# Optimization experiments

Measured on AMD Instinct MI355X. Metric: run time of the kernel, lower is better.

Reference implementation:

```python
import jax, jax.numpy as jnp
import numpy as np

B, S, D, H = 4, 1024, 1024, 16
DH = D // H  # head dim 64
DFF = 4 * D


def _lin(x, w, b):
    # torch nn.Linear: x @ W^T + b, W: [out, in]
    return x @ w.T + b


def _heads(x):
    # [B,S,D] -> [B,H,S,DH]
    b, s, _ = x.shape
    return x.reshape(b, s, H, DH).transpose(0, 2, 1, 3)


def setup_inputs() -> dict:
    key = jax.random.key(0)
    ks = iter(jax.random.split(key, 32))

    def w(shape):
        return jax.random.normal(next(ks), shape, jnp.float32) * 0.02

    inp = {
        "global_feat": jax.random.normal(next(ks), (B, S, D), jnp.float32),
        "local_feat": jax.random.normal(next(ks), (B, S, D), jnp.float32),
        "text_feat": jax.random.normal(next(ks), (B, S, D), jnp.float32),
    }
    # embedding blocks (build) and all projections: D x D linears
    for name in ["ge", "le1", "le2", "qg", "kg", "vg", "qp", "kp", "vp", "dense", "ml"]:
        inp[name + "_w"] = w((D, D))
        inp[name + "_b"] = w((D,))
    # MLP: D -> 4D -> D
    inp["fc1_w"] = w((DFF, D)); inp["fc1_b"] = w((DFF,))
    inp["fc2_w"] = w((D, DFF)); inp["fc2_b"] = w((D,))
    return inp


def reference(global_feat, local_feat, text_feat,
              ge_w, ge_b, le1_w, le1_b, le2_w, le2_b,
              qg_w, qg_b, kg_w, kg_b, vg_w, vg_b,
              qp_w, qp_b, kp_w, kp_b, vp_w, vp_b,
              dense_w, dense_b, ml_w, ml_b,
              fc1_w, fc1_b, fc2_w, fc2_b):
    b, s, d = global_feat.shape
    scale = 1.0 / jnp.sqrt(jnp.asarray(DH, global_feat.dtype))

    # embeddings (build blocks; dropout = identity in eval)
    dup_local = _lin(local_feat, le1_w, le1_b)
    local = _lin(local_feat, le2_w, le2_b)
    glob = _lin(global_feat, ge_w, ge_b)

    # global branch: Q from global, K/V from local
    qg = _heads(_lin(glob, qg_w, qg_b))
    kg = _heads(_lin(local, kg_w, kg_b))
    vg = _heads(_lin(local, vg_w, vg_b))
    # local branch: Q from duplicated local, K/V from text
    qp = _heads(_lin(dup_local, qp_w, qp_b))
    kp = _heads(_lin(text_feat, kp_w, kp_b))
    vp = _heads(_lin(text_feat, vp_w, vp_b))

    glb_probs = jax.nn.softmax(jnp.einsum("bhqd,bhkd->bhqk", qg, kg) * scale, axis=-1)
    plb_probs = jax.nn.softmax(jnp.einsum("bhqd,bhkd->bhqk", qp, kp) * scale, axis=-1)

    # bridge: probs @ probs (the non-standard O(S^3) stage)
    plb_enh = jnp.einsum("bhqk,bhks->bhqs", glb_probs, plb_probs)

    glb_ctx = jnp.einsum("bhqk,bhkd->bhqd", glb_probs, vg)
    plb_ctx = jnp.einsum("bhqs,bhsd->bhqd", plb_enh, vp)

    def merge(x):
        return x.transpose(0, 2, 1, 3).reshape(b, s, d)

    last = merge(glb_ctx) + merge(plb_ctx)
    out = _lin(last, dense_w, dense_b)
    # MLP: D -> 4D -> D with GELU
    out = _lin(jax.nn.gelu(_lin(out, fc1_w, fc1_b), approximate=False), fc2_w, fc2_b)
    out = _lin(out, ml_w, ml_b)
    return out
```

## Files before the change

kernel.cpp:

```cpp
#include <hip/hip_runtime.h>
#include <cstdint>
#include <cstddef>

#define B_   4
#define S_   1024
#define D_   1024
#define H_   16
#define DH_  64
#define DFF_ 4096
#define M_   (B_ * S_)

typedef __bf16 bf16x8 __attribute__((ext_vector_type(8)));
typedef float  f32x4  __attribute__((ext_vector_type(4)));

__device__ __forceinline__ unsigned short f2bf(float f) {
  unsigned int u = __float_as_uint(f);
  u = (u + 0x7fffu + ((u >> 16) & 1u)) >> 16;
  return (unsigned short)u;
}

__device__ __forceinline__ float bf2f(unsigned short h) {
  return __uint_as_float(((unsigned int)h) << 16);
}

__device__ __forceinline__ void gload_lds16(const void* g, void* l) {
  __builtin_amdgcn_global_load_lds((const __attribute__((address_space(1))) void*)g,
                                   (__attribute__((address_space(3))) void*)l, 16, 0, 0);
}

#define NCVT 16
struct CvtB { const float* s[NCVT]; unsigned short* d[NCVT]; int n[NCVT]; };

__global__ __launch_bounds__(256)
void cvt_k(CvtB cb) {
  const int z = blockIdx.y;
  const float* __restrict__ s = cb.s[z];
  unsigned short* __restrict__ d = cb.d[z];
  const int n = cb.n[z];
  const int stride = gridDim.x * 256 * 4;
  for (int i = (blockIdx.x * 256 + threadIdx.x) * 4; i < n; i += stride) {
    const float4 v = *(const float4*)(s + i);
    const unsigned int a = (unsigned int)f2bf(v.x) | ((unsigned int)f2bf(v.y) << 16);
    const unsigned int b = (unsigned int)f2bf(v.z) | ((unsigned int)f2bf(v.w) << 16);
    *(uint2*)(d + i) = make_uint2(a, b);
  }
}

#define MAXB 6
struct GemmB {
  const unsigned short* A[MAXB];
  const unsigned short* W[MAXB];
  const float*          bias[MAXB];
  void*                 Y[MAXB];
};

template <int GELU, int OUTF32>
__global__ __launch_bounds__(256)
void mgemm(GemmB gb, int M, int N, int K) {
  __shared__ unsigned short sA0[128][32], sA1[128][32];
  __shared__ unsigned short sB0[128][32], sB1[128][32];

  const int z = blockIdx.z;
  const unsigned short* __restrict__ A = gb.A[z];
  const unsigned short* __restrict__ W = gb.W[z];
  const float* __restrict__ bias = gb.bias[z];

  const int t  = threadIdx.x;
  const int ln = t & 63;
  const int wv = t >> 6;
  const int wr = wv >> 1;
  const int wc = wv & 1;

  const int gx   = gridDim.x;
  const int nwg  = gx * gridDim.y;
  const int orig = blockIdx.y * gx + blockIdx.x;
  const int q8   = nwg >> 3, r8 = nwg & 7;
  const int xcd  = orig & 7, idx = orig >> 3;
  const int wgid = (xcd < r8 ? xcd * (q8 + 1) : r8 * (q8 + 1) + (xcd - r8) * q8) + idx;
  const int m0 = (wgid / gx) * 128;
  const int n0 = (wgid % gx) * 128;

  const int srow  = ln >> 2;
  const int skoff = (ln & 3) << 3;

  f32x4 acc[4][4] = {};

  char* a0 = (char*)&sA0[0][0];  char* a1 = (char*)&sA1[0][0];
  char* b0 = (char*)&sB0[0][0];  char* b1 = (char*)&sB1[0][0];

  const int rsel = ln & 15;
  const int csel = (ln >> 4) << 4;

  auto stage = [&](int kt, char* dstA, char* dstB) {
    const int k0 = kt << 5;
#pragma unroll
    for (int i = 0; i < 2; ++i) {
      const int c = (wv << 1) | i;
      gload_lds16(A + (size_t)(m0 + (c << 4) + srow) * K + k0 + skoff, dstA + (c << 10));
      gload_lds16(W + (size_t)(n0 + (c << 4) + srow) * K + k0 + skoff, dstB + (c << 10));
    }
  };

  auto compute = [&](const char* srcA, const char* srcB) {
    bf16x8 av[4], bv[4];
#pragma unroll
    for (int m = 0; m < 4; ++m)
      av[m] = *(const bf16x8*)(srcA + (((wr << 6) + (m << 4) + rsel) << 6) + csel);
#pragma unroll
    for (int n = 0; n < 4; ++n)
      bv[n] = *(const bf16x8*)(srcB + (((wc << 6) + (n << 4) + rsel) << 6) + csel);
#pragma unroll
    for (int m = 0; m < 4; ++m)
#pragma unroll
      for (int n = 0; n < 4; ++n)
        acc[m][n] = __builtin_amdgcn_mfma_f32_16x16x32_bf16(av[m], bv[n], acc[m][n], 0, 0, 0);
  };

  const int NK = K >> 5;
  stage(0, a0, b0);
  for (int kt = 0; kt < NK; kt += 2) {
    __syncthreads();
    stage(kt + 1, a1, b1);
    compute(a0, b0);
    __syncthreads();
    if (kt + 2 < NK) stage(kt + 2, a0, b0);
    compute(a1, b1);
  }

  const int rbase = m0 + (wr << 6) + ((ln >> 4) << 2);
  const int cb0   = n0 + (wc << 6) + (ln & 15);
#pragma unroll
  for (int m = 0; m < 4; ++m) {
#pragma unroll
    for (int n = 0; n < 4; ++n) {
      const int col = cb0 + (n << 4);
      const float bi = bias[col];
#pragma unroll
      for (int j = 0; j < 4; ++j) {
        const int row = rbase + (m << 4) + j;
        float x = acc[m][n][j] + bi;
        if (GELU) x = 0.5f * x * (1.0f + erff(x * 0.70710678118654752f));
        if (OUTF32) ((float*)gb.Y[z])[(size_t)row * N + col] = x;
        else        ((unsigned short*)gb.Y[z])[(size_t)row * N + col] = f2bf(x);
      }
    }
  }
}

__global__ __launch_bounds__(256)
void vtrans_k(const unsigned short* __restrict__ V, unsigned short* __restrict__ Vt) {
  const int t   = threadIdx.x;
  const int d   = t & 63;
  const int sub = t >> 6;
  const int bh  = blockIdx.y;
  const int b   = bh >> 4;
  const int col0 = (bh & 15) * DH_;
  const int kv0 = blockIdx.x * 32 + sub * 8;
  unsigned short tmp[8];
#pragma unroll
  for (int i = 0; i < 8; ++i)
    tmp[i] = V[((size_t)b * S_ + kv0 + i) * D_ + col0 + d];
  *(uint4*)(Vt + ((size_t)bh * DH_ + d) * S_ + kv0) = *(const uint4*)tmp;
}

__global__ __launch_bounds__(256)
void attn_mfma_k(const unsigned short* __restrict__ Q,
                 const unsigned short* __restrict__ K,
                 const unsigned short* __restrict__ Vt,
                 const unsigned short* __restrict__ addend,
                 unsigned short* __restrict__ O) {
  __shared__ unsigned short sQ[64 * 64];
  __shared__ unsigned short sK[64 * 64];
  __shared__ unsigned short sV[64 * 64];
  __shared__ unsigned short sP[4][16 * 72];

  const int t  = threadIdx.x;
  const int l  = t & 63;
  const int w  = t >> 6;
  const int bh = blockIdx.y;
  const int b  = bh >> 4;
  const size_t rowQ = (size_t)b * S_ + blockIdx.x * 64;
  const size_t rowK = (size_t)b * S_;
  const int col0 = (bh & 15) * DH_;

  const int lr8 = l >> 3;
  const int lsw = (l & 7) ^ lr8;
  char* sQb = (char*)sQ;
  char* sKb = (char*)sK;
  char* sVb = (char*)sV;

#pragma unroll
  for (int i = 0; i < 2; ++i) {
    const int r = w * 16 + i * 8 + lr8;
    gload_lds16(Q + (rowQ + r) * D_ + col0 + lsw * 8, sQb + w * 2048 + i * 1024);
    gload_lds16(K + (rowK + r) * D_ + col0 + lsw * 8, sKb + w * 2048 + i * 1024);
    gload_lds16(Vt + ((size_t)bh * DH_ + r) * S_ + lsw * 8, sVb + w * 2048 + i * 1024);
  }
  __syncthreads();

  bf16x8 qa[2];
#pragma unroll
  for (int c = 0; c < 2; ++c)
    qa[c] = *(const bf16x8*)(sQb + (w * 16 + (l & 15)) * 128 +
                             ((((c << 2) + (l >> 4)) ^ (l & 7)) << 4));

  f32x4 o[4] = {};
  float mrow[4] = {-1e30f, -1e30f, -1e30f, -1e30f};
  float lrow[4] = {0.f, 0.f, 0.f, 0.f};

  char* sPw = (char*)(sP[w]);

  for (int kt = 0; kt < S_ / 64; ++kt) {
    f32x4 s[4];
#pragma unroll
    for (int n = 0; n < 4; ++n) {
      f32x4 z = {};
#pragma unroll
      for (int c = 0; c < 2; ++c) {
        const bf16x8 kb = *(const bf16x8*)(sKb + (n * 16 + (l & 15)) * 128 +
                              ((((c << 2) + (l >> 4)) ^ (l & 7)) << 4));
        z = __builtin_amdgcn_mfma_f32_16x16x32_bf16(qa[c], kb, z, 0, 0, 0);
      }
      s[n] = z;
    }

#pragma unroll
    for (int j = 0; j < 4; ++j) {
      float rm = fmaxf(fmaxf(s[0][j], s[1][j]), fmaxf(s[2][j], s[3][j]));
      rm = fmaxf(rm, __shfl_xor(rm, 1));
      rm = fmaxf(rm, __shfl_xor(rm, 2));
      rm = fmaxf(rm, __shfl_xor(rm, 4));
      rm = fmaxf(rm, __shfl_xor(rm, 8));
      const float mn = fmaxf(mrow[j], rm * 0.125f);
      const float cr = __expf(mrow[j] - mn);
      mrow[j] = mn;
      float rs = 0.f;
#pragma unroll
      for (int n = 0; n < 4; ++n) {
        const float p = __expf(s[n][j] * 0.125f - mn);
        rs += p;
        ((unsigned short*)sPw)[((l >> 4) * 4 + j) * 72 + n * 16 + (l & 15)] = f2bf(p);
      }
      rs += __shfl_xor(rs, 1);
      rs += __shfl_xor(rs, 2);
      rs += __shfl_xor(rs, 4);
      rs += __shfl_xor(rs, 8);
      lrow[j] = lrow[j] * cr + rs;
#pragma unroll
      for (int n2 = 0; n2 < 4; ++n2) o[n2][j] *= cr;
    }

    bf16x8 pa[2];
#pragma unroll
    for (int kc = 0; kc < 2; ++kc)
      pa[kc] = *(const bf16x8*)(sPw + (l & 15) * 144 + kc * 64 + (l >> 4) * 16);
#pragma unroll
    for (int n2 = 0; n2 < 4; ++n2) {
#pragma unroll
      for (int kc = 0; kc < 2; ++kc) {
        const bf16x8 vb = *(const bf16x8*)(sVb + (n2 * 16 + (l & 15)) * 128 +
                               ((((kc << 2) + (l >> 4)) ^ (l & 7)) << 4));
        o[n2] = __builtin_amdgcn_mfma_f32_16x16x32_bf16(pa[kc], vb, o[n2], 0, 0, 0);
      }
    }

    __syncthreads();
    if (kt + 1 < S_ / 64) {
#pragma unroll
      for (int i = 0; i < 2; ++i) {
        const int r = w * 16 + i * 8 + lr8;
        gload_lds16(K + (rowK + (size_t)(kt + 1) * 64 + r) * D_ + col0 + lsw * 8,
                    sKb + w * 2048 + i * 1024);
        gload_lds16(Vt + ((size_t)bh * DH_ + r) * S_ + (kt + 1) * 64 + lsw * 8,
                    sVb + w * 2048 + i * 1024);
      }
    }
    __syncthreads();
  }

  float inv[4];
#pragma unroll
  for (int j = 0; j < 4; ++j) inv[j] = 1.f / lrow[j];
#pragma unroll
  for (int n2 = 0; n2 < 4; ++n2) {
#pragma unroll
    for (int j = 0; j < 4; ++j) {
      const size_t row = rowQ + w * 16 + (l >> 4) * 4 + j;
      const int col = col0 + n2 * 16 + (l & 15);
      float x = o[n2][j] * inv[j];
      if (addend != nullptr) x += bf2f(addend[row * D_ + col]);
      O[row * D_ + col] = f2bf(x);
    }
  }
}

extern "C" void kernel_launch(void* const* d_in, const int* in_sizes, int n_in,
                              void* d_out, int out_size, void* d_ws, size_t ws_size,
                              hipStream_t stream) {
  const float* gf = (const float*)d_in[0];
  const float* lf = (const float*)d_in[1];
  const float* tf = (const float*)d_in[2];
  const float* ge_w  = (const float*)d_in[3],  *ge_b  = (const float*)d_in[4];
  const float* le1_w = (const float*)d_in[5],  *le1_b = (const float*)d_in[6];
  const float* le2_w = (const float*)d_in[7],  *le2_b = (const float*)d_in[8];
  const float* qg_w  = (const float*)d_in[9],  *qg_b  = (const float*)d_in[10];
  const float* kg_w  = (const float*)d_in[11], *kg_b  = (const float*)d_in[12];
  const float* vg_w  = (const float*)d_in[13], *vg_b  = (const float*)d_in[14];
  const float* qp_w  = (const float*)d_in[15], *qp_b  = (const float*)d_in[16];
  const float* kp_w  = (const float*)d_in[17], *kp_b  = (const float*)d_in[18];
  const float* vp_w  = (const float*)d_in[19], *vp_b  = (const float*)d_in[20];
  const float* dense_w = (const float*)d_in[21], *dense_b = (const float*)d_in[22];
  const float* ml_w  = (const float*)d_in[23], *ml_b  = (const float*)d_in[24];
  const float* fc1_w = (const float*)d_in[25], *fc1_b = (const float*)d_in[26];
  const float* fc2_w = (const float*)d_in[27], *fc2_b = (const float*)d_in[28];

  float* out = (float*)d_out;

  char* p = (char*)d_ws;
  auto take = [&](size_t bytes) { char* r = p; p += (bytes + 255) & ~(size_t)255; return r; };
  const size_t WD  = (size_t)D_ * D_;
  const size_t WF  = (size_t)DFF_ * D_;
  const size_t ACT = (size_t)M_ * D_;
  const size_t HB  = (size_t)M_ * DFF_;

  unsigned short* wge    = (unsigned short*)take(WD * 2);
  unsigned short* wle1   = (unsigned short*)take(WD * 2);
  unsigned short* wle2   = (unsigned short*)take(WD * 2);
  unsigned short* wqg    = (unsigned short*)take(WD * 2);
  unsigned short* wkg    = (unsigned short*)take(WD * 2);
  unsigned short* wvg    = (unsigned short*)take(WD * 2);
  unsigned short* wqp    = (unsigned short*)take(WD * 2);
  unsigned short* wkp    = (unsigned short*)take(WD * 2);
  unsigned short* wvp    = (unsigned short*)take(WD * 2);
  unsigned short* wdense = (unsigned short*)take(WD * 2);
  unsigned short* wml    = (unsigned short*)take(WD * 2);
  unsigned short* wfc1   = (unsigned short*)take(WF * 2);
  unsigned short* wfc2   = (unsigned short*)take(WF * 2);
  unsigned short* gfb    = (unsigned short*)take(ACT * 2);
  unsigned short* lfb    = (unsigned short*)take(ACT * 2);
  unsigned short* tfb    = (unsigned short*)take(ACT * 2);
  unsigned short* glob   = (unsigned short*)take(ACT * 2);
  unsigned short* loc    = (unsigned short*)take(ACT * 2);
  unsigned short* dup    = (unsigned short*)take(ACT * 2);
  unsigned short* qgb    = (unsigned short*)take(ACT * 2);
  unsigned short* kgb    = (unsigned short*)take(ACT * 2);
  unsigned short* vgb    = (unsigned short*)take(ACT * 2);
  unsigned short* qpb    = (unsigned short*)take(ACT * 2);
  unsigned short* kpb    = (unsigned short*)take(ACT * 2);
  unsigned short* vpb    = (unsigned short*)take(ACT * 2);
  unsigned short* ub     = (unsigned short*)take(ACT * 2);
  unsigned short* lastb  = (unsigned short*)take(ACT * 2);
  unsigned short* out1   = (unsigned short*)take(ACT * 2);
  unsigned short* hbuf   = (unsigned short*)take(HB * 2);
  unsigned short* out2   = (unsigned short*)take(ACT * 2);

  unsigned short* vt1 = gfb;
  unsigned short* vtu = lfb;

  CvtB cb;
  const float* srcs[NCVT] = {ge_w, le1_w, le2_w, qg_w, kg_w, vg_w, qp_w, kp_w, vp_w,
                             dense_w, ml_w, fc1_w, fc2_w, gf, lf, tf};
  unsigned short* dsts[NCVT] = {wge, wle1, wle2, wqg, wkg, wvg, wqp, wkp, wvp,
                                wdense, wml, wfc1, wfc2, gfb, lfb, tfb};
  const int lens[NCVT] = {(int)WD,(int)WD,(int)WD,(int)WD,(int)WD,(int)WD,(int)WD,(int)WD,(int)WD,
                          (int)WD,(int)WD,(int)WF,(int)WF,(int)ACT,(int)ACT,(int)ACT};
  for (int i = 0; i < NCVT; ++i) { cb.s[i] = srcs[i]; cb.d[i] = dsts[i]; cb.n[i] = lens[i]; }
  hipLaunchKernelGGL(cvt_k, dim3(512, NCVT), dim3(256), 0, stream, cb);

  const dim3 blk(256);
  auto mkb = [](std::initializer_list<const unsigned short*> As,
                std::initializer_list<const unsigned short*> Ws,
                std::initializer_list<const float*> Bs,
                std::initializer_list<void*> Ys) {
    GemmB g{};
    int i = 0;
    auto a = As.begin(); auto w = Ws.begin(); auto b = Bs.begin(); auto y = Ys.begin();
    for (; a != As.end(); ++a, ++w, ++b, ++y, ++i) { g.A[i] = *a; g.W[i] = *w; g.bias[i] = *b; g.Y[i] = *y; }
    return g;
  };

  GemmB s1 = mkb({gfb, lfb, lfb}, {wge, wle1, wle2}, {ge_b, le1_b, le2_b},
                 {glob, dup, loc});
  hipLaunchKernelGGL((mgemm<0,0>), dim3(D_/128, M_/128, 3), blk, 0, stream, s1, M_, D_, D_);

  GemmB s2 = mkb({glob, loc, loc, dup, tfb, tfb}, {wqg, wkg, wvg, wqp, wkp, wvp},
                 {qg_b, kg_b, vg_b, qp_b, kp_b, vp_b}, {qgb, kgb, vgb, qpb, kpb, vpb});
  hipLaunchKernelGGL((mgemm<0,0>), dim3(D_/128, M_/128, 6), blk, 0, stream, s2, M_, D_, D_);

  hipLaunchKernelGGL(vtrans_k, dim3(32, 64), blk, 0, stream, vpb, vt1);
  hipLaunchKernelGGL(attn_mfma_k, dim3(16, 64), blk, 0, stream, qpb, kpb, vt1, vgb, ub);
  hipLaunchKernelGGL(vtrans_k, dim3(32, 64), blk, 0, stream, ub, vtu);
  hipLaunchKernelGGL(attn_mfma_k, dim3(16, 64), blk, 0, stream, qgb, kgb, vtu,
                     (const unsigned short*)nullptr, lastb);

  GemmB gd = mkb({lastb}, {wdense}, {dense_b}, {out1});
  hipLaunchKernelGGL((mgemm<0,0>), dim3(D_/128, M_/128, 1), blk, 0, stream, gd, M_, D_, D_);
  GemmB g1 = mkb({out1}, {wfc1}, {fc1_b}, {hbuf});
  hipLaunchKernelGGL((mgemm<1,0>), dim3(DFF_/128, M_/128, 1), blk, 0, stream, g1, M_, DFF_, D_);
  GemmB g2 = mkb({hbuf}, {wfc2}, {fc2_b}, {out2});
  hipLaunchKernelGGL((mgemm<0,0>), dim3(D_/128, M_/128, 1), blk, 0, stream, g2, M_, D_, DFF_);
  GemmB gm = mkb({out2}, {wml}, {ml_b}, {out});
  hipLaunchKernelGGL((mgemm<0,1>), dim3(D_/128, M_/128, 1), blk, 0, stream, gm, M_, D_, D_);
}
```

Before: 599.4 us.

## Fold embedding linears into projection weights and double-buffer attention K/V tiles

Since the embedding linears feed straight into the Q/K/V projections, the code now precomputes combined weights (Wq·We) with a small 1024x1024 GEMM and combined biases (Wq·be + bq). The separate 3-way embedding GEMM stage and its intermediate activations go away, so the projections read the converted input features directly. This removes a full M×D×D GEMM pass over three outputs, at the cost of a few weight-sized GEMMs, a transpose kernel and some bf16 rounding of the fused weights. The attention kernel also gets double-buffered K/V shared-memory tiles, so the next tile loads while the current one is computed.

```diff
diff --git a/kernel.cpp b/kernel.cpp
--- a/kernel.cpp
+++ b/kernel.cpp
@@ -46,6 +46,50 @@
   }
 }
 
+struct WtB { const float* s[3]; unsigned short* d[3]; };
+
+__global__ __launch_bounds__(256)
+void wtrans_k(WtB wb) {
+  const int z = blockIdx.z;
+  const float* __restrict__ S = wb.s[z];
+  unsigned short* __restrict__ T = wb.d[z];
+  const int t = threadIdx.x;
+  const int dcol = blockIdx.y * 64 + (t & 63);
+  const int r0   = blockIdx.x * 32 + (t >> 6) * 8;
+  unsigned short tmp[8];
+#pragma unroll
+  for (int i = 0; i < 8; ++i)
+    tmp[i] = f2bf(S[(size_t)(r0 + i) * 1024 + dcol]);
+  *(uint4*)(T + (size_t)dcol * 1024 + r0) = *(const uint4*)tmp;
+}
+
+struct BcB { const float* w[4]; const float* eb[4]; const float* pb[4]; float* o[4]; };
+
+__global__ __launch_bounds__(256)
+void bcomp_k(BcB bb) {
+  const int z = blockIdx.y;
+  const float* __restrict__ Wp = bb.w[z];
+  const float* __restrict__ be = bb.eb[z];
+  const float* __restrict__ pb = bb.pb[z];
+  float* __restrict__ o = bb.o[z];
+  const int w = threadIdx.x >> 6, l = threadIdx.x & 63;
+  for (int pass = 0; pass < 16; ++pass) {
+    const int n = blockIdx.x * 64 + pass * 4 + w;
+    const float* row = Wp + (size_t)n * 1024 + l * 16;
+    float acc = 0.f;
+#pragma unroll
+    for (int i = 0; i < 4; ++i) {
+      const float4 a = *(const float4*)(row + i * 4);
+      const float4 b = *(const float4*)(be + l * 16 + i * 4);
+      acc += a.x * b.x + a.y * b.y + a.z * b.z + a.w * b.w;
+    }
+    acc += __shfl_xor(acc, 1);  acc += __shfl_xor(acc, 2);
+    acc += __shfl_xor(acc, 4);  acc += __shfl_xor(acc, 8);
+    acc += __shfl_xor(acc, 16); acc += __shfl_xor(acc, 32);
+    if (l == 0) o[n] = acc + pb[n];
+  }
+}
+
 #define MAXB 6
 struct GemmB {
   const unsigned short* A[MAXB];
@@ -54,7 +98,7 @@
   void*                 Y[MAXB];
 };
 
-template <int GELU, int OUTF32>
+template <int GELU, int OUTF32, int NB>
 __global__ __launch_bounds__(256)
 void mgemm(GemmB gb, int M, int N, int K) {
   __shared__ unsigned short sA0[128][32], sA1[128][32];
@@ -134,7 +178,7 @@
 #pragma unroll
     for (int n = 0; n < 4; ++n) {
       const int col = cb0 + (n << 4);
-      const float bi = bias[col];
+      const float bi = NB ? 0.f : bias[col];
 #pragma unroll
       for (int j = 0; j < 4; ++j) {
         const int row = rbase + (m << 4) + j;
@@ -170,8 +214,8 @@
                  const unsigned short* __restrict__ addend,
                  unsigned short* __restrict__ O) {
   __shared__ unsigned short sQ[64 * 64];
-  __shared__ unsigned short sK[64 * 64];
-  __shared__ unsigned short sV[64 * 64];
+  __shared__ unsigned short sK0[64 * 64], sK1[64 * 64];
+  __shared__ unsigned short sV0[64 * 64], sV1[64 * 64];
   __shared__ unsigned short sP[4][16 * 72];
 
   const int t  = threadIdx.x;
@@ -185,43 +229,47 @@
 
   const int lr8 = l >> 3;
   const int lsw = (l & 7) ^ lr8;
-  char* sQb = (char*)sQ;
-  char* sKb = (char*)sK;
-  char* sVb = (char*)sV;
+
+  auto stageKV = [&](int kt, char* dK, char* dV) {
+#pragma unroll
+    for (int i = 0; i < 2; ++i) {
+      const int r = w * 16 + i * 8 + lr8;
+      gload_lds16(K + (rowK + (size_t)kt * 64 + r) * D_ + col0 + lsw * 8, dK + w * 2048 + i * 1024);
+      gload_lds16(Vt + ((size_t)bh * DH_ + r) * S_ + kt * 64 + lsw * 8, dV + w * 2048 + i * 1024);
+    }
+  };
 
 #pragma unroll
   for (int i = 0; i < 2; ++i) {
     const int r = w * 16 + i * 8 + lr8;
-    gload_lds16(Q + (rowQ + r) * D_ + col0 + lsw * 8, sQb + w * 2048 + i * 1024);
-    gload_lds16(K + (rowK + r) * D_ + col0 + lsw * 8, sKb + w * 2048 + i * 1024);
-    gload_lds16(Vt + ((size_t)bh * DH_ + r) * S_ + lsw * 8, sVb + w * 2048 + i * 1024);
-  }
+    gload_lds16(Q + (rowQ + r) * D_ + col0 + lsw * 8, (char*)sQ + w * 2048 + i * 1024);
+  }
+  stageKV(0, (char*)sK0, (char*)sV0);
   __syncthreads();
 
   bf16x8 qa[2];
 #pragma unroll
   for (int c = 0; c < 2; ++c)
-    qa[c] = *(const bf16x8*)(sQb + (w * 16 + (l & 15)) * 128 +
+    qa[c] = *(const bf16x8*)((char*)sQ + (w * 16 + (l & 15)) * 128 +
                              ((((c << 2) + (l >> 4)) ^ (l & 7)) << 4));
 
   f32x4 o[4] = {};
   float mrow[4] = {-1e30f, -1e30f, -1e30f, -1e30f};
   float lrow[4] = {0.f, 0.f, 0.f, 0.f};
-
   char* sPw = (char*)(sP[w]);
 
-  for (int kt = 0; kt < S_ / 64; ++kt) {
+  auto tile = [&](const char* sKb, const char* sVb) {
     f32x4 s[4];
 #pragma unroll
     for (int n = 0; n < 4; ++n) {
-      f32x4 z = {};
+      f32x4 zz = {};
 #pragma unroll
       for (int c = 0; c < 2; ++c) {
         const bf16x8 kb = *(const bf16x8*)(sKb + (n * 16 + (l & 15)) * 128 +
                               ((((c << 2) + (l >> 4)) ^ (l & 7)) << 4));
-        z = __builtin_amdgcn_mfma_f32_16x16x32_bf16(qa[c], kb, z, 0, 0, 0);
+        zz = __builtin_amdgcn_mfma_f32_16x16x32_bf16(qa[c], kb, zz, 0, 0, 0);
       }
-      s[n] = z;
+      s[n] = zz;
     }
 
 #pragma unroll
@@ -263,18 +311,14 @@
         o[n2] = __builtin_amdgcn_mfma_f32_16x16x32_bf16(pa[kc], vb, o[n2], 0, 0, 0);
       }
     }
-
+  };
+
+  for (int kt = 0; kt < S_ / 64; kt += 2) {
+    if (kt + 1 < S_ / 64) stageKV(kt + 1, (char*)sK1, (char*)sV1);
+    tile((char*)sK0, (char*)sV0);
     __syncthreads();
-    if (kt + 1 < S_ / 64) {
-#pragma unroll
-      for (int i = 0; i < 2; ++i) {
-        const int r = w * 16 + i * 8 + lr8;
-        gload_lds16(K + (rowK + (size_t)(kt + 1) * 64 + r) * D_ + col0 + lsw * 8,
-                    sKb + w * 2048 + i * 1024);
-        gload_lds16(Vt + ((size_t)bh * DH_ + r) * S_ + (kt + 1) * 64 + lsw * 8,
-                    sVb + w * 2048 + i * 1024);
-      }
-    }
+    if (kt + 2 < S_ / 64) stageKV(kt + 2, (char*)sK0, (char*)sV0);
+    tile((char*)sK1, (char*)sV1);
     __syncthreads();
   }
 
@@ -323,9 +367,6 @@
   const size_t ACT = (size_t)M_ * D_;
   const size_t HB  = (size_t)M_ * DFF_;
 
-  unsigned short* wge    = (unsigned short*)take(WD * 2);
-  unsigned short* wle1   = (unsigned short*)take(WD * 2);
-  unsigned short* wle2   = (unsigned short*)take(WD * 2);
   unsigned short* wqg    = (unsigned short*)take(WD * 2);
   unsigned short* wkg    = (unsigned short*)take(WD * 2);
   unsigned short* wvg    = (unsigned short*)take(WD * 2);
@@ -336,12 +377,20 @@
   unsigned short* wml    = (unsigned short*)take(WD * 2);
   unsigned short* wfc1   = (unsigned short*)take(WF * 2);
   unsigned short* wfc2   = (unsigned short*)take(WF * 2);
+  unsigned short* geT    = (unsigned short*)take(WD * 2);
+  unsigned short* le1T   = (unsigned short*)take(WD * 2);
+  unsigned short* le2T   = (unsigned short*)take(WD * 2);
+  unsigned short* cWqg   = (unsigned short*)take(WD * 2);
+  unsigned short* cWkg   = (unsigned short*)take(WD * 2);
+  unsigned short* cWvg   = (unsigned short*)take(WD * 2);
+  unsigned short* cWqp   = (unsigned short*)take(WD * 2);
+  float* cbqg = (float*)take(D_ * 4);
+  float* cbkg = (float*)take(D_ * 4);
+  float* cbvg = (float*)take(D_ * 4);
+  float* cbqp = (float*)take(D_ * 4);
   unsigned short* gfb    = (unsigned short*)take(ACT * 2);
   unsigned short* lfb    = (unsigned short*)take(ACT * 2);
   unsigned short* tfb    = (unsigned short*)take(ACT * 2);
-  unsigned short* glob   = (unsigned short*)take(ACT * 2);
-  unsigned short* loc    = (unsigned short*)take(ACT * 2);
-  unsigned short* dup    = (unsigned short*)take(ACT * 2);
   unsigned short* qgb    = (unsigned short*)take(ACT * 2);
   unsigned short* kgb    = (unsigned short*)take(ACT * 2);
   unsigned short* vgb    = (unsigned short*)take(ACT * 2);
@@ -358,14 +407,14 @@
   unsigned short* vtu = lfb;
 
   CvtB cb;
-  const float* srcs[NCVT] = {ge_w, le1_w, le2_w, qg_w, kg_w, vg_w, qp_w, kp_w, vp_w,
-                             dense_w, ml_w, fc1_w, fc2_w, gf, lf, tf};
-  unsigned short* dsts[NCVT] = {wge, wle1, wle2, wqg, wkg, wvg, wqp, wkp, wvp,
-                                wdense, wml, wfc1, wfc2, gfb, lfb, tfb};
-  const int lens[NCVT] = {(int)WD,(int)WD,(int)WD,(int)WD,(int)WD,(int)WD,(int)WD,(int)WD,(int)WD,
-                          (int)WD,(int)WD,(int)WF,(int)WF,(int)ACT,(int)ACT,(int)ACT};
-  for (int i = 0; i < NCVT; ++i) { cb.s[i] = srcs[i]; cb.d[i] = dsts[i]; cb.n[i] = lens[i]; }
-  hipLaunchKernelGGL(cvt_k, dim3(512, NCVT), dim3(256), 0, stream, cb);
+  const float* srcs[13] = {qg_w, kg_w, vg_w, qp_w, kp_w, vp_w,
+                           dense_w, ml_w, fc1_w, fc2_w, gf, lf, tf};
+  unsigned short* dsts[13] = {wqg, wkg, wvg, wqp, wkp, wvp,
+                              wdense, wml, wfc1, wfc2, gfb, lfb, tfb};
+  const int lens[13] = {(int)WD,(int)WD,(int)WD,(int)WD,(int)WD,(int)WD,
+                        (int)WD,(int)WD,(int)WF,(int)WF,(int)ACT,(int)ACT,(int)ACT};
+  for (int i = 0; i < 13; ++i) { cb.s[i] = srcs[i]; cb.d[i] = dsts[i]; cb.n[i] = lens[i]; }
+  hipLaunchKernelGGL(cvt_k, dim3(512, 13), dim3(256), 0, stream, cb);
 
   const dim3 blk(256);
   auto mkb = [](std::initializer_list<const unsigned short*> As,
@@ -379,13 +428,28 @@
     return g;
   };
 
-  GemmB s1 = mkb({gfb, lfb, lfb}, {wge, wle1, wle2}, {ge_b, le1_b, le2_b},
-                 {glob, dup, loc});
-  hipLaunchKernelGGL((mgemm<0,0>), dim3(D_/128, M_/128, 3), blk, 0, stream, s1, M_, D_, D_);
-
-  GemmB s2 = mkb({glob, loc, loc, dup, tfb, tfb}, {wqg, wkg, wvg, wqp, wkp, wvp},
-                 {qg_b, kg_b, vg_b, qp_b, kp_b, vp_b}, {qgb, kgb, vgb, qpb, kpb, vpb});
-  hipLaunchKernelGGL((mgemm<0,0>), dim3(D_/128, M_/128, 6), blk, 0, stream, s2, M_, D_, D_);
+  WtB wt;
+  wt.s[0] = ge_w; wt.s[1] = le1_w; wt.s[2] = le2_w;
+  wt.d[0] = geT;  wt.d[1] = le1T;  wt.d[2] = le2T;
+  hipLaunchKernelGGL(wtrans_k, dim3(32, 16, 3), blk, 0, stream, wt);
+
+  BcB bc;
+  bc.w[0] = qg_w; bc.eb[0] = ge_b;  bc.pb[0] = qg_b; bc.o[0] = cbqg;
+  bc.w[1] = kg_w; bc.eb[1] = le2_b; bc.pb[1] = kg_b; bc.o[1] = cbkg;
+  bc.w[2] = vg_w; bc.eb[2] = le2_b; bc.pb[2] = vg_b; bc.o[2] = cbvg;
+  bc.w[3] = qp_w; bc.eb[3] = le1_b; bc.pb[3] = qp_b; bc.o[3] = cbqp;
+  hipLaunchKernelGGL(bcomp_k, dim3(16, 4), blk, 0, stream, bc);
+
+  GemmB wc = mkb({wqg, wkg, wvg, wqp}, {geT, le2T, le2T, le1T},
+                 {ge_b, ge_b, ge_b, ge_b},
+                 {cWqg, cWkg, cWvg, cWqp});
+  hipLaunchKernelGGL((mgemm<0,0,1>), dim3(D_/128, D_/128, 4), blk, 0, stream, wc, D_, D_, D_);
+
+  GemmB s2 = mkb({gfb, lfb, lfb, lfb, tfb, tfb},
+                 {cWqg, cWkg, cWvg, cWqp, wkp, wvp},
+                 {cbqg, cbkg, cbvg, cbqp, kp_b, vp_b},
+                 {qgb, kgb, vgb, qpb, kpb, vpb});
+  hipLaunchKernelGGL((mgemm<0,0,0>), dim3(D_/128, M_/128, 6), blk, 0, stream, s2, M_, D_, D_);
 
   hipLaunchKernelGGL(vtrans_k, dim3(32, 64), blk, 0, stream, vpb, vt1);
   hipLaunchKernelGGL(attn_mfma_k, dim3(16, 64), blk, 0, stream, qpb, kpb, vt1, vgb, ub);
@@ -394,11 +458,11 @@
                      (const unsigned short*)nullptr, lastb);
 
   GemmB gd = mkb({lastb}, {wdense}, {dense_b}, {out1});
-  hipLaunchKernelGGL((mgemm<0,0>), dim3(D_/128, M_/128, 1), blk, 0, stream, gd, M_, D_, D_);
+  hipLaunchKernelGGL((mgemm<0,0,0>), dim3(D_/128, M_/128, 1), blk, 0, stream, gd, M_, D_, D_);
   GemmB g1 = mkb({out1}, {wfc1}, {fc1_b}, {hbuf});
-  hipLaunchKernelGGL((mgemm<1,0>), dim3(DFF_/128, M_/128, 1), blk, 0, stream, g1, M_, DFF_, D_);
+  hipLaunchKernelGGL((mgemm<1,0,0>), dim3(DFF_/128, M_/128, 1), blk, 0, stream, g1, M_, DFF_, D_);
   GemmB g2 = mkb({hbuf}, {wfc2}, {fc2_b}, {out2});
-  hipLaunchKernelGGL((mgemm<0,0>), dim3(D_/128, M_/128, 1), blk, 0, stream, g2, M_, D_, DFF_);
+  hipLaunchKernelGGL((mgemm<0,0,0>), dim3(D_/128, M_/128, 1), blk, 0, stream, g2, M_, D_, DFF_);
   GemmB gm = mkb({out2}, {wml}, {ml_b}, {out});
-  hipLaunchKernelGGL((mgemm<0,1>), dim3(D_/128, M_/128, 1), blk, 0, stream, gm, M_, D_, D_);
-}
+  hipLaunchKernelGGL((mgemm<0,1,0>), dim3(D_/128, M_/128, 1), blk, 0, stream, gm, M_, D_, D_);
+}
```

Result: no change. 599.6 us (+0.0%).
